# Optimization experiments

Measured on AMD Instinct MI355X. Metric: run time of the kernel, lower is better.

## Reference

```python
import jax, jax.numpy as jnp
import numpy as np

SIGMA = 1.0
RADIUS = 3          # Gaussian kernel radius -> kernel size 7
TAU = 1.0
ITERATIONS = 20
EPS = 1e-6


def _gauss_kernel_1d(sigma: float, radius: int) -> jnp.ndarray:
    x = jnp.arange(-radius, radius + 1, dtype=jnp.float32)
    k = jnp.exp(-0.5 * (x / sigma) ** 2)
    return k / k.sum()


def _smooth(v: jnp.ndarray, k1d: jnp.ndarray) -> jnp.ndarray:
    """Separable Gaussian smoothing of a (1, C, D, H, W) field, 'same' padding."""
    C = v.shape[1]
    r = (k1d.size - 1) // 2
    for ax in range(3):
        shape = [1, 1, 1]
        shape[ax] = k1d.size
        ker = jnp.tile(k1d.reshape((1, 1) + tuple(shape)), (C, 1, 1, 1, 1))
        pad = [(r, r) if i == ax else (0, 0) for i in range(3)]
        v = jax.lax.conv_general_dilated(
            v, ker, window_strides=(1, 1, 1), padding=pad,
            dimension_numbers=('NCDHW', 'OIDHW', 'NCDHW'),
            feature_group_count=C)
    return v


def _warp(image: jnp.ndarray, disp: jnp.ndarray) -> jnp.ndarray:
    """Trilinear warp of (1,1,D,H,W) image by voxel displacement (1,3,D,H,W)."""
    D, H, W = image.shape[2:]
    gd, gh, gw = jnp.meshgrid(
        jnp.arange(D, dtype=disp.dtype),
        jnp.arange(H, dtype=disp.dtype),
        jnp.arange(W, dtype=disp.dtype), indexing='ij')
    coords = [gd + disp[0, 0], gh + disp[0, 1], gw + disp[0, 2]]
    warped = jax.scipy.ndimage.map_coordinates(image[0, 0], coords, order=1, mode='nearest')
    return warped[None, None]


def _spatial_gradient(img: jnp.ndarray) -> jnp.ndarray:
    # img: (D, H, W) -> (3, D, H, W), central differences
    return jnp.stack(jnp.gradient(img))


def _demon_forces_dual(warped, fixed, fixed_grad):
    # warped/fixed: (1,1,D,H,W); dual gradient = mean of moving/fixed gradients
    diff = (warped - fixed)[0, 0]                      # (D,H,W)
    g = 0.5 * (_spatial_gradient(warped[0, 0]) + fixed_grad)  # (3,D,H,W)
    denom = (g ** 2).sum(axis=0) + diff ** 2           # (D,H,W)
    f = jnp.where(denom > EPS, diff * g / denom, 0.0)  # (3,D,H,W)
    return f[None]                                     # (1,3,D,H,W)


def setup_inputs() -> dict:
    key = jax.random.key(0)
    k1, k2 = jax.random.split(key)
    shape = (1, 1, 128, 128, 128)
    moving_image = jax.random.uniform(k1, shape, dtype=jnp.float32)
    fixed_image = jax.random.uniform(k2, shape, dtype=jnp.float32)
    return {"moving_image": moving_image, "fixed_image": fixed_image}


def reference(moving_image, fixed_image):
    kernel = _gauss_kernel_1d(SIGMA, RADIUS)
    fixed_grad = _spatial_gradient(fixed_image[0, 0])
    vf0 = jnp.zeros((1, 3) + moving_image.shape[2:], dtype=moving_image.dtype)

    def step(vf, _):
        warped = _warp(moving_image, vf)
        forces = _demon_forces_dual(warped, fixed_image, fixed_grad)
        vf = _smooth(vf + TAU * forces, kernel)
        return vf, None

    vf, _ = jax.lax.scan(step, vf0, None, length=ITERATIONS)
    return vf
```

## Files before the change

### kernel.cpp

```cpp
#include <hip/hip_runtime.h>
#include <hip/hip_cooperative_groups.h>

namespace cg = cooperative_groups;

static constexpr int DIM = 128;
static constexpr int N = DIM * DIM * DIM;
static constexpr int ITERS = 20;
static constexpr float EPS = 1e-6f;

#define W0 0.39905028f
#define W1 0.24203624f
#define W2 0.05400559f
#define W3 0.00443305f

__device__ __forceinline__ int clamp_i(int v, int lo, int hi) {
    return min(max(v, lo), hi);
}

#define ROWS 22
#define SSTR 132
#define SC(c, r) ((((c) * ROWS) + (r)) * SSTR)
#define LDS_FLOATS (3 * ROWS * SSTR)

__device__ __forceinline__ void forces_phase(const float* __restrict__ wpd,
                                             const float* __restrict__ fix,
                                             const float* __restrict__ vf,
                                             float* __restrict__ u2,
                                             float* S, bool first, int b) {
    int z  = b >> 3;
    int y0 = (b & 7) << 4;

    for (int e = threadIdx.x; e < ROWS * 32; e += 256) {
        int x4 = e & 31;
        int r  = e >> 5;
        int gy = y0 + r - 3;
        float4 rz = make_float4(0, 0, 0, 0);
        float4 ry = make_float4(0, 0, 0, 0);
        float4 rx = make_float4(0, 0, 0, 0);
        if (gy >= 0 && gy < 128) {
            int idx = (z << 14) + (gy << 7) + (x4 << 2);
            int xb = x4 << 2;

            float4 wc4 = *(const float4*)(wpd + idx);
            float4 fc4 = *(const float4*)(fix + idx);

            int iyp = (gy < 127) ? idx + 128   : idx;
            int iym = (gy > 0)   ? idx - 128   : idx;
            int izp = (z < 127)  ? idx + 16384 : idx;
            int izm = (z > 0)    ? idx - 16384 : idx;

            float4 wyp = *(const float4*)(wpd + iyp), wym = *(const float4*)(wpd + iym);
            float4 wzp = *(const float4*)(wpd + izp), wzm = *(const float4*)(wpd + izm);
            float4 fyp = *(const float4*)(fix + iyp), fym = *(const float4*)(fix + iym);
            float4 fzp = *(const float4*)(fix + izp), fzm = *(const float4*)(fix + izm);

            float wl = __shfl_up(wc4.w, 1);
            float wr = __shfl_down(wc4.x, 1);
            float fl = __shfl_up(fc4.w, 1);
            float fr = __shfl_down(fc4.x, 1);

            float wcv[4] = {wc4.x, wc4.y, wc4.z, wc4.w};
            float fcv[4] = {fc4.x, fc4.y, fc4.z, fc4.w};
            float wypv[4] = {wyp.x, wyp.y, wyp.z, wyp.w};
            float wymv[4] = {wym.x, wym.y, wym.z, wym.w};
            float wzpv[4] = {wzp.x, wzp.y, wzp.z, wzp.w};
            float wzmv[4] = {wzm.x, wzm.y, wzm.z, wzm.w};
            float fypv[4] = {fyp.x, fyp.y, fyp.z, fyp.w};
            float fymv[4] = {fym.x, fym.y, fym.z, fym.w};
            float fzpv[4] = {fzp.x, fzp.y, fzp.z, fzp.w};
            float fzmv[4] = {fzm.x, fzm.y, fzm.z, fzm.w};

            float4 vz4 = first ? make_float4(0, 0, 0, 0) : *(const float4*)(vf + idx);
            float4 vy4 = first ? make_float4(0, 0, 0, 0) : *(const float4*)(vf + N + idx);
            float4 vx4 = first ? make_float4(0, 0, 0, 0) : *(const float4*)(vf + 2 * N + idx);
            float vzv[4] = {vz4.x, vz4.y, vz4.z, vz4.w};
            float vyv[4] = {vy4.x, vy4.y, vy4.z, vy4.w};
            float vxv[4] = {vx4.x, vx4.y, vx4.z, vx4.w};

            float ozv[4], oyv[4], oxv[4];
#pragma unroll
            for (int i = 0; i < 4; ++i) {
                float wc = wcv[i], fc = fcv[i];
                float diff = wc - fc;

                float gwz = (z == 0)   ? (wzpv[i] - wc)
                          : (z == 127) ? (wc - wzmv[i])
                          : 0.5f * (wzpv[i] - wzmv[i]);
                float gfz = (z == 0)   ? (fzpv[i] - fc)
                          : (z == 127) ? (fc - fzmv[i])
                          : 0.5f * (fzpv[i] - fzmv[i]);
                float grz = 0.5f * (gwz + gfz);

                float gwy = (gy == 0)   ? (wypv[i] - wc)
                          : (gy == 127) ? (wc - wymv[i])
                          : 0.5f * (wypv[i] - wymv[i]);
                float gfy = (gy == 0)   ? (fypv[i] - fc)
                          : (gy == 127) ? (fc - fymv[i])
                          : 0.5f * (fypv[i] - fymv[i]);
                float gry = 0.5f * (gwy + gfy);

                float wleft  = (i == 0) ? wl : wcv[i - 1];
                float wright = (i == 3) ? wr : wcv[i + 1];
                float fleft  = (i == 0) ? fl : fcv[i - 1];
                float fright = (i == 3) ? fr : fcv[i + 1];
                int xi = xb + i;
                float gwx = (xi == 0)   ? (wright - wc)
                          : (xi == 127) ? (wc - wleft)
                          : 0.5f * (wright - wleft);
                float gfx = (xi == 0)   ? (fright - fc)
                          : (xi == 127) ? (fc - fleft)
                          : 0.5f * (fright - fleft);
                float grx = 0.5f * (gwx + gfx);

                float denom = grz * grz + gry * gry + grx * grx + diff * diff;
                float s = (denom > EPS) ? (diff / denom) : 0.0f;
                ozv[i] = vzv[i] + s * grz;
                oyv[i] = vyv[i] + s * gry;
                oxv[i] = vxv[i] + s * grx;
            }
            rz = make_float4(ozv[0], ozv[1], ozv[2], ozv[3]);
            ry = make_float4(oyv[0], oyv[1], oyv[2], oyv[3]);
            rx = make_float4(oxv[0], oxv[1], oxv[2], oxv[3]);
        }

        float4 vch[3] = {rz, ry, rx};
#pragma unroll
        for (int c = 0; c < 3; ++c) {
            float4 v0 = vch[c];
            float4 m1, p1;
            m1.x = __shfl_up(v0.x, 1);  m1.y = __shfl_up(v0.y, 1);
            m1.z = __shfl_up(v0.z, 1);  m1.w = __shfl_up(v0.w, 1);
            p1.x = __shfl_down(v0.x, 1); p1.y = __shfl_down(v0.y, 1);
            p1.z = __shfl_down(v0.z, 1); p1.w = __shfl_down(v0.w, 1);
            if (x4 == 0)  m1 = make_float4(0, 0, 0, 0);
            if (x4 == 31) p1 = make_float4(0, 0, 0, 0);
            float w[12] = {m1.x, m1.y, m1.z, m1.w,
                           v0.x, v0.y, v0.z, v0.w,
                           p1.x, p1.y, p1.z, p1.w};
            float o[4];
#pragma unroll
            for (int i = 0; i < 4; ++i) {
                o[i] = W3 * (w[i + 1] + w[i + 7]) + W2 * (w[i + 2] + w[i + 6])
                     + W1 * (w[i + 3] + w[i + 5]) + W0 * w[i + 4];
            }
            *(float4*)(S + SC(c, r) + (x4 << 2)) = make_float4(o[0], o[1], o[2], o[3]);
        }
    }
    __syncthreads();

    for (int e = threadIdx.x; e < 16 * 32 * 3; e += 256) {
        int x4 = e & 31;
        int t2 = e >> 5;
        int y  = t2 & 15;
        int c  = t2 >> 4;
        const float* base = S + SC(c, y) + (x4 << 2);
        float4 v0 = *(const float4*)(base);
        float4 v1 = *(const float4*)(base + 1 * SSTR);
        float4 v2 = *(const float4*)(base + 2 * SSTR);
        float4 v3 = *(const float4*)(base + 3 * SSTR);
        float4 v4 = *(const float4*)(base + 4 * SSTR);
        float4 v5 = *(const float4*)(base + 5 * SSTR);
        float4 v6 = *(const float4*)(base + 6 * SSTR);
        float4 acc;
        acc.x = W3 * (v0.x + v6.x) + W2 * (v1.x + v5.x) + W1 * (v2.x + v4.x) + W0 * v3.x;
        acc.y = W3 * (v0.y + v6.y) + W2 * (v1.y + v5.y) + W1 * (v2.y + v4.y) + W0 * v3.y;
        acc.z = W3 * (v0.z + v6.z) + W2 * (v1.z + v5.z) + W1 * (v2.z + v4.z) + W0 * v3.z;
        acc.w = W3 * (v0.w + v6.w) + W2 * (v1.w + v5.w) + W1 * (v2.w + v4.w) + W0 * v3.w;
        *(float4*)(u2 + (size_t)c * N + ((size_t)z << 14) + ((y0 + y) << 7) + (x4 << 2)) = acc;
    }
}

__device__ __forceinline__ void zblur_phase(const float* __restrict__ u2,
                                            const float* __restrict__ mov,
                                            float* __restrict__ vf,
                                            float* __restrict__ warped,
                                            bool do_warp, int b) {
    int k  = b & 7;
    int j  = b >> 3;
    int lb = ((j & 15) << 6) + (k << 3) + (j >> 4);
    int g  = lb * 256 + threadIdx.x;
    int col = g & 16383;
    int zc  = g >> 14;
    int z0  = zc << 3;
    int x = col & 127, y = col >> 7;

    float bz[3][8];
#pragma unroll
    for (int c = 0; c < 3; ++c) {
        const float* inp = u2 + (size_t)c * N + col;
        float win[14];
#pragma unroll
        for (int i = 0; i < 14; ++i) {
            int zz = z0 - 3 + i;
            win[i] = (zz >= 0 && zz < 128) ? inp[(size_t)zz << 14] : 0.0f;
        }
#pragma unroll
        for (int k8 = 0; k8 < 8; ++k8) {
            bz[c][k8] = W3 * (win[k8] + win[k8 + 6]) + W2 * (win[k8 + 1] + win[k8 + 5])
                      + W1 * (win[k8 + 2] + win[k8 + 4]) + W0 * win[k8 + 3];
        }
        float* outp = vf + (size_t)c * N + col;
#pragma unroll
        for (int k8 = 0; k8 < 8; ++k8)
            outp[(size_t)(z0 + k8) << 14] = bz[c][k8];
    }

    if (do_warp) {
        for (int k8 = 0; k8 < 8; ++k8) {
            int z = z0 + k8;
            float cz = (float)z + bz[0][k8];
            float cy = (float)y + bz[1][k8];
            float cx = (float)x + bz[2][k8];

            float flz = floorf(cz), fly = floorf(cy), flx = floorf(cx);
            float fz = cz - flz, fy = cy - fly, fx = cx - flx;

            int zi = (int)flz, yi = (int)fly, xi = (int)flx;
            int z0c = clamp_i(zi, 0, DIM - 1), z1c = clamp_i(zi + 1, 0, DIM - 1);
            int y0c = clamp_i(yi, 0, DIM - 1), y1c = clamp_i(yi + 1, 0, DIM - 1);
            int x0c = clamp_i(xi, 0, DIM - 1), x1c = clamp_i(xi + 1, 0, DIM - 1);

            int b00 = (z0c << 14) + (y0c << 7);
            int b01 = (z0c << 14) + (y1c << 7);
            int b10 = (z1c << 14) + (y0c << 7);
            int b11 = (z1c << 14) + (y1c << 7);

            float v000 = mov[b00 + x0c], v001 = mov[b00 + x1c];
            float v010 = mov[b01 + x0c], v011 = mov[b01 + x1c];
            float v100 = mov[b10 + x0c], v101 = mov[b10 + x1c];
            float v110 = mov[b11 + x0c], v111 = mov[b11 + x1c];

            float c00 = v000 + fx * (v001 - v000);
            float c01 = v010 + fx * (v011 - v010);
            float c10 = v100 + fx * (v101 - v100);
            float c11 = v110 + fx * (v111 - v110);
            float c0 = c00 + fy * (c01 - c00);
            float c1 = c10 + fy * (c11 - c10);
            warped[((size_t)z << 14) + col] = c0 + fz * (c1 - c0);
        }
    }
}

__global__ __launch_bounds__(256, 4) void demons_persistent(const float* mov,
                                                            const float* fix,
                                                            float* vf,
                                                            float* warped,
                                                            float* u2) {
    cg::grid_group grid = cg::this_grid();
    __shared__ float S[LDS_FLOATS];
    int b = blockIdx.x;

    for (int it = 0; it < ITERS; ++it) {
        bool first = (it == 0);
        forces_phase(first ? mov : warped, fix, vf, u2, S, first, b);
        grid.sync();
        zblur_phase(u2, mov, vf, warped, it < ITERS - 1, b);
        if (it < ITERS - 1) grid.sync();
    }
}

template <bool FIRST>
__global__ __launch_bounds__(256, 4) void forces_xy_kernel(const float* __restrict__ wpd,
                                                           const float* __restrict__ fix,
                                                           const float* __restrict__ vf,
                                                           float* __restrict__ u2) {
    __shared__ float S[LDS_FLOATS];
    forces_phase(wpd, fix, vf, u2, S, FIRST, blockIdx.x);
}

template <bool DO_WARP>
__global__ __launch_bounds__(256, 4) void zblur_warp_kernel(const float* __restrict__ u2,
                                                            const float* __restrict__ mov,
                                                            float* __restrict__ vf,
                                                            float* __restrict__ warped) {
    zblur_phase(u2, mov, vf, warped, DO_WARP, blockIdx.x);
}

extern "C" void kernel_launch(void* const* d_in, const int* in_sizes, int n_in,
                              void* d_out, int out_size, void* d_ws, size_t ws_size,
                              hipStream_t stream) {
    const float* mov = (const float*)d_in[0];
    const float* fix = (const float*)d_in[1];
    float* vf = (float*)d_out;
    float* ws = (float*)d_ws;
    float* warped = ws;
    float* u2     = ws + (size_t)N;

    const int BLK = 256;
    const int GRID = 1024;

    static int coop_ok = -1;
    if (coop_ok < 0) {
        int dev = 0;
        (void)hipGetDevice(&dev);
        int coop = 0;
        (void)hipDeviceGetAttribute(&coop, hipDeviceAttributeCooperativeLaunch, dev);
        int ncu = 0;
        (void)hipDeviceGetAttribute(&ncu, hipDeviceAttributeMultiprocessorCount, dev);
        int occ = 0;
        (void)hipOccupancyMaxActiveBlocksPerMultiprocessor(&occ, demons_persistent, BLK, 0);
        coop_ok = (coop && (long long)occ * ncu >= GRID) ? 1 : 0;
    }

    if (coop_ok) {
        void* args[] = {(void*)&mov, (void*)&fix, (void*)&vf, (void*)&warped, (void*)&u2};
        (void)hipLaunchCooperativeKernel(demons_persistent, dim3(GRID), dim3(BLK),
                                         args, 0, stream);
    } else {
        forces_xy_kernel<true><<<GRID, BLK, 0, stream>>>(mov, fix, nullptr, u2);
        zblur_warp_kernel<true><<<GRID, BLK, 0, stream>>>(u2, mov, vf, warped);
        for (int it = 1; it < ITERS - 1; ++it) {
            forces_xy_kernel<false><<<GRID, BLK, 0, stream>>>(warped, fix, vf, u2);
            zblur_warp_kernel<true><<<GRID, BLK, 0, stream>>>(u2, mov, vf, warped);
        }
        forces_xy_kernel<false><<<GRID, BLK, 0, stream>>>(warped, fix, vf, u2);
        zblur_warp_kernel<false><<<GRID, BLK, 0, stream>>>(u2, mov, vf, warped);
    }
}
```

Measured before the change: 766.6 us.

## Replace grid-wide barriers with neighbor-slab atomic counter waits

```diff
diff --git a/kernel.cpp b/kernel.cpp
--- a/kernel.cpp
+++ b/kernel.cpp
@@ -241,21 +241,54 @@
     }
 }
 
+__device__ __forceinline__ void wait_ge(unsigned int* c, unsigned int target) {
+    while (__hip_atomic_load(c, __ATOMIC_ACQUIRE, __HIP_MEMORY_SCOPE_AGENT) < target)
+        __builtin_amdgcn_s_sleep(1);
+}
+
 __global__ __launch_bounds__(256, 4) void demons_persistent(const float* mov,
                                                             const float* fix,
                                                             float* vf,
                                                             float* warped,
-                                                            float* u2) {
+                                                            float* u2,
+                                                            unsigned int* cnt) {
     cg::grid_group grid = cg::this_grid();
     __shared__ float S[LDS_FLOATS];
     int b = blockIdx.x;
+    int s = b & 7;
+    unsigned int* cntA = cnt;
+    unsigned int* cntB = cnt + 8;
+
+    if (b == 0 && threadIdx.x < 16) cnt[threadIdx.x] = 0u;
+    grid.sync();
 
     for (int it = 0; it < ITERS; ++it) {
         bool first = (it == 0);
+        if (!first) {
+            if (threadIdx.x == 0) {
+                unsigned int tgt = (unsigned int)it * 128u;
+                if (s > 0) wait_ge(&cntB[s - 1], tgt);
+                wait_ge(&cntB[s], tgt);
+                if (s < 7) wait_ge(&cntB[s + 1], tgt);
+            }
+            __syncthreads();
+        }
         forces_phase(first ? mov : warped, fix, vf, u2, S, first, b);
-        grid.sync();
+        __syncthreads();
+        if (threadIdx.x == 0) {
+            __hip_atomic_fetch_add(&cntA[s], 1u, __ATOMIC_RELEASE, __HIP_MEMORY_SCOPE_AGENT);
+            unsigned int tgt = (unsigned int)(it + 1) * 128u;
+            if (s > 0) wait_ge(&cntA[s - 1], tgt);
+            wait_ge(&cntA[s], tgt);
+            if (s < 7) wait_ge(&cntA[s + 1], tgt);
+        }
+        __syncthreads();
         zblur_phase(u2, mov, vf, warped, it < ITERS - 1, b);
-        if (it < ITERS - 1) grid.sync();
+        if (it < ITERS - 1) {
+            __syncthreads();
+            if (threadIdx.x == 0)
+                __hip_atomic_fetch_add(&cntB[s], 1u, __ATOMIC_RELEASE, __HIP_MEMORY_SCOPE_AGENT);
+        }
     }
 }
 
@@ -285,6 +318,7 @@
     float* ws = (float*)d_ws;
     float* warped = ws;
     float* u2     = ws + (size_t)N;
+    unsigned int* cnt = (unsigned int*)(ws + (size_t)4 * N);
 
     const int BLK = 256;
     const int GRID = 1024;
@@ -299,11 +333,13 @@
         (void)hipDeviceGetAttribute(&ncu, hipDeviceAttributeMultiprocessorCount, dev);
         int occ = 0;
         (void)hipOccupancyMaxActiveBlocksPerMultiprocessor(&occ, demons_persistent, BLK, 0);
-        coop_ok = (coop && (long long)occ * ncu >= GRID) ? 1 : 0;
+        coop_ok = (coop && (long long)occ * ncu >= GRID &&
+                   ws_size >= (size_t)4 * N * sizeof(float) + 64) ? 1 : 0;
     }
 
     if (coop_ok) {
-        void* args[] = {(void*)&mov, (void*)&fix, (void*)&vf, (void*)&warped, (void*)&u2};
+        void* args[] = {(void*)&mov, (void*)&fix, (void*)&vf, (void*)&warped,
+                        (void*)&u2, (void*)&cnt};
         (void)hipLaunchCooperativeKernel(demons_persistent, dim3(GRID), dim3(BLK),
                                          args, 0, stream);
     } else {
```

Measured after the change: 766.9 us. No clear change (+0.0%).
